# Optimization experiments

Hardware: AMD Instinct MI355X
Metric: run time of the kernel (lower is better)

## Reference

```python
import jax, jax.numpy as jnp
import numpy as np

B, C, H, W = 8, 128, 128, 128

def setup_inputs() -> dict:
    key = jax.random.key(0)
    ks = jax.random.split(key, 6)
    s = 1.0 / np.sqrt(C)
    return {
        "x": jax.random.normal(ks[0], (B, C, H, W), dtype=jnp.float32),
        "w_qkv": jax.random.uniform(ks[1], (3 * C, C), jnp.float32, -s, s),
        "w_gate": jax.random.uniform(ks[2], (C, C), jnp.float32, -s, s),
        "b_gate": jax.random.uniform(ks[3], (C,), jnp.float32, -s, s),
        "w_proj": jax.random.uniform(ks[4], (C, C), jnp.float32, -s, s),
        "b_proj": jax.random.uniform(ks[5], (C,), jnp.float32, -s, s),
    }

def reference(x, w_qkv, w_gate, b_gate, w_proj, b_proj):
    b, c, h, w = x.shape
    n = h * w
    # [b,c,h,w] -> [b,n,c]
    x_seq = jnp.transpose(x, (0, 2, 3, 1)).reshape(b, n, c)
    # SiLU gate on spatial-domain features
    t = jax.nn.silu(x_seq @ w_gate.T + b_gate)  # [b,n,c]
    x_sp = x_seq.reshape(b, h, w, c)
    # frequency domain (ortho norm carries the 1/N factor)
    x_fft = jnp.fft.rfft2(x_sp, axes=(1, 2), norm="ortho")  # [b,h,w//2+1,c] complex64
    # complex linear with real weight == apply weight to real & imag parts
    qkv = jnp.einsum("bhwc,dc->bhwd", x_fft, w_qkv.astype(x_fft.dtype))
    q, k, v = jnp.split(qkv, 3, axis=-1)
    # eq.15: a = F^{-1}(conj(F(Q)) * F(K))
    attn = jnp.fft.irfft2(jnp.conj(q) * k, s=(h, w), axes=(1, 2), norm="ortho")
    # softmax over the flattened spatial axis n
    attn = jax.nn.softmax(attn.reshape(b, n, c), axis=1).reshape(b, h, w, c)
    # eq.16: O = F^{-1}(conj(F(sigma(a))) * F(V)); note forward rfft2 uses default (backward) norm
    attn_f = jnp.fft.rfft2(attn, axes=(1, 2))
    out = jnp.fft.irfft2(jnp.conj(attn_f) * v, s=(h, w), axes=(1, 2), norm="ortho")
    out = out.reshape(b, n, c) * t
    out = out @ w_proj.T + b_proj
    return jnp.transpose(out.reshape(b, h, w, c), (0, 3, 1, 2))
```

## Files before the change

### kernel.cpp

```cpp
#include <hip/hip_runtime.h>
#include <math.h>


constexpr int CH    = 128;
constexpr int NSP   = 128 * 128;
constexpr int BATCH = 8;
constexpr int NIMG  = BATCH * CH;
constexpr int RS    = 130;
constexpr int NT    = 1024;
constexpr int NW    = NT / 64;


typedef short short8 __attribute__((ext_vector_type(8)));
typedef float f32x4  __attribute__((ext_vector_type(4)));
union U8 { unsigned u[4]; short8 s; };

__device__ __forceinline__ unsigned bf16r(float x) {
  unsigned u = __float_as_uint(x);
  return (u + 0x7FFFu + ((u >> 16) & 1u)) >> 16;
}
__device__ __forceinline__ float bflo(unsigned w) { return __uint_as_float(w << 16); }
__device__ __forceinline__ float bfhi(unsigned w) { return __uint_as_float(w & 0xFFFF0000u); }

__device__ __forceinline__ void split_pair(float e0, float e1,
                                           unsigned& hi, unsigned& lo) {
  const unsigned u0 = __float_as_uint(e0), u1 = __float_as_uint(e1);
  hi = (u0 >> 16) | (u1 & 0xFFFF0000u);
  const float r0 = e0 - __uint_as_float(u0 & 0xFFFF0000u);
  const float r1 = e1 - __uint_as_float(u1 & 0xFFFF0000u);
  lo = bf16r(r0) | (bf16r(r1) << 16);
}

__device__ __forceinline__ void load_a_frag(const float* wr, short8& ah, short8& al) {
  const float4 wa = *(const float4*)wr;
  const float4 wb = *(const float4*)(wr + 4);
  U8 hi, lo;
  split_pair(wa.x, wa.y, hi.u[0], lo.u[0]);
  split_pair(wa.z, wa.w, hi.u[1], lo.u[1]);
  split_pair(wb.x, wb.y, hi.u[2], lo.u[2]);
  split_pair(wb.z, wb.w, hi.u[3], lo.u[3]);
  ah = hi.s; al = lo.s;
}


__global__ void prep_weights(const float* __restrict__ w_qkv,
                             const float* __restrict__ w_gate,
                             const float* __restrict__ w_proj,
                             short* __restrict__ wpre) {
  const int t = blockIdx.x * 256 + threadIdx.x;
  const int lane = t & 63;
  const int mf   = (t >> 6) & 3;
  const int kg   = (t >> 8) & 3;
  const int mbi  = (t >> 10) & 1;
  const int g    = t >> 11;
  if (g >= 5) return;
  const float* W = (g < 3) ? (w_qkv + (size_t)g * CH * CH)
                           : (g == 3 ? w_gate : w_proj);
  const int row = mbi * 64 + mf * 16 + (lane & 15);
  const int k0  = kg * 32 + (lane >> 4) * 8;
  short8 ah, al;
  load_a_frag(W + (size_t)row * CH + k0, ah, al);
  const size_t base = ((size_t)(g * 2 + mbi) * 16 + kg * 4 + mf) * 1024;
  *(short8*)(wpre + base + lane * 8)       = ah;
  *(short8*)(wpre + base + 512 + lane * 8) = al;
}


__device__ __forceinline__ void mfma_half(const short8* __restrict__ wf,
                                          const short8 bh[4], const short8 bl[4],
                                          f32x4 acc[4][4], int kg, int lane) {
  short8 ah[4], al[4];
#pragma unroll
  for (int mf = 0; mf < 4; ++mf) {
    const short8* p = wf + (kg * 4 + mf) * 128 + lane;
    ah[mf] = p[0];
    al[mf] = p[64];
  }
#pragma unroll
  for (int mf = 0; mf < 4; ++mf)
#pragma unroll
    for (int nf = 0; nf < 4; ++nf)
      acc[mf][nf] = __builtin_amdgcn_mfma_f32_16x16x32_bf16(al[mf], bh[nf], acc[mf][nf], 0, 0, 0);
#pragma unroll
  for (int mf = 0; mf < 4; ++mf)
#pragma unroll
    for (int nf = 0; nf < 4; ++nf)
      acc[mf][nf] = __builtin_amdgcn_mfma_f32_16x16x32_bf16(ah[mf], bl[nf], acc[mf][nf], 0, 0, 0);
#pragma unroll
  for (int mf = 0; mf < 4; ++mf)
#pragma unroll
    for (int nf = 0; nf < 4; ++nf)
      acc[mf][nf] = __builtin_amdgcn_mfma_f32_16x16x32_bf16(ah[mf], bh[nf], acc[mf][nf], 0, 0, 0);
}

__device__ __forceinline__ void mfma_core2(const unsigned* xs,
                                           const short8* __restrict__ wfA,
                                           const short8* __restrict__ wfB,
                                           f32x4 aA[4][4], f32x4 aB[4][4], int tid) {
  const int lane = tid & 63, wid = tid >> 6;
  const int nb = (wid & 1) * 64;
  const int lm = lane & 15, quad = lane >> 4;
#pragma unroll
  for (int kg = 0; kg < 4; ++kg) {
    short8 bh[4], bl[4];
    const int kwb = (kg * 16 + quad * 4) ^ (lm << 2);
#pragma unroll
    for (int nf = 0; nf < 4; ++nf) {
      const unsigned* p = xs + (nb + nf * 16 + lm) * 64 + kwb;
      bh[nf] = *(const short8*)p;
      bl[nf] = *(const short8*)(p + 8192);
    }
    mfma_half(wfA, bh, bl, aA, kg, lane);
    mfma_half(wfB, bh, bl, aB, kg, lane);
  }
}

__device__ __forceinline__ void mfma_core1(const unsigned* xs,
                                           const short8* __restrict__ wf,
                                           f32x4 acc[4][4], int tid) {
  const int lane = tid & 63, wid = tid >> 6;
  const int nb = (wid & 1) * 64;
  const int lm = lane & 15, quad = lane >> 4;
#pragma unroll
  for (int kg = 0; kg < 4; ++kg) {
    short8 bh[4], bl[4];
    const int kwb = (kg * 16 + quad * 4) ^ (lm << 2);
#pragma unroll
    for (int nf = 0; nf < 4; ++nf) {
      const unsigned* p = xs + (nb + nf * 16 + lm) * 64 + kwb;
      bh[nf] = *(const short8*)p;
      bl[nf] = *(const short8*)(p + 8192);
    }
    mfma_half(wf, bh, bl, acc, kg, lane);
  }
}


__global__ __launch_bounds__(256, 2)
void gemm_qkvg(const float* __restrict__ x, const short* __restrict__ wpre,
               const float* __restrict__ b_gate,
               unsigned* __restrict__ QKp, unsigned short* __restrict__ Vp,
               float* __restrict__ Tp) {
  __shared__ __align__(16) unsigned xs[16384];
  __shared__ __align__(16) float bounce[4 * 528];
  const int tid = threadIdx.x;
  const int n0 = blockIdx.x * 128;
  const int b  = blockIdx.y;
  const float* xb = x + (size_t)b * CH * NSP;

  {
    const int tn = tid >> 3;
    const int tk = tid & 7;
#pragma unroll
    for (int i = 0; i < 8; ++i) {
      const int k = 2 * tk + 16 * i;
      const float* p0 = xb + (size_t)k * NSP + n0 + 4 * tn;
      const float4 a = *(const float4*)p0;
      const float4 c = *(const float4*)(p0 + NSP);
      const float a4[4] = {a.x, a.y, a.z, a.w};
      const float c4[4] = {c.x, c.y, c.z, c.w};
      const int kw = tk + 8 * i;
#pragma unroll
      for (int j = 0; j < 4; ++j) {
        const int nn = 4 * tn + j;
        unsigned hi, lo;
        split_pair(a4[j], c4[j], hi, lo);
        const int kws = kw ^ ((nn & 15) << 2);
        xs[nn * 64 + kws] = hi;
        xs[8192 + nn * 64 + kws] = lo;
      }
    }
  }
  __syncthreads();

  const int lane = tid & 63, wid = tid >> 6;
  const int mb = (wid >> 1) * 64, nb = (wid & 1) * 64;
  const int lm = lane & 15, quad = lane >> 4;
  const int mbi = wid >> 1;
  const short8* wp = (const short8*)wpre;
  const short8* wQ = wp + (size_t)(0 * 2 + mbi) * 2048;
  const short8* wK = wp + (size_t)(1 * 2 + mbi) * 2048;
  const short8* wV = wp + (size_t)(2 * 2 + mbi) * 2048;
  const short8* wG = wp + (size_t)(3 * 2 + mbi) * 2048;
  float* const bw = bounce + wid * 528;
  unsigned* const ubw = (unsigned*)bw;

  f32x4 aq[4][4], ak[4][4];
#pragma unroll
  for (int mf = 0; mf < 4; ++mf)
#pragma unroll
    for (int nf = 0; nf < 4; ++nf) { aq[mf][nf] = (f32x4){0,0,0,0}; ak[mf][nf] = (f32x4){0,0,0,0}; }
  mfma_core2(xs, wQ, wK, aq, ak, tid);

#pragma unroll
  for (int mf = 0; mf < 4; ++mf) {
#pragma unroll
    for (int half = 0; half < 2; ++half) {
#pragma unroll
      for (int nn = 0; nn < 2; ++nn) {
        const int nf = half * 2 + nn;
#pragma unroll
        for (int i = 0; i < 4; ++i)
          ubw[(quad * 4 + i) * 33 + nn * 16 + lm] =
              bf16r(aq[mf][nf][i]) | (bf16r(ak[mf][nf][i]) << 16);
      }
#pragma unroll
      for (int j = 0; j < 2; ++j) {
        const int rl = (lane >> 3) + 8 * j;
        const int cl = (lane & 7) * 4;
        const uint4 v = *(const uint4*)(ubw + rl * 33 + cl);
        const int row = mb + mf * 16 + rl;
        *(uint4*)(QKp + ((size_t)b * CH + row) * NSP + n0 + nb + half * 32 + cl) = v;
      }
    }
  }

  f32x4 av[4][4], at[4][4];
#pragma unroll
  for (int mf = 0; mf < 4; ++mf)
#pragma unroll
    for (int nf = 0; nf < 4; ++nf) { av[mf][nf] = (f32x4){0,0,0,0}; at[mf][nf] = (f32x4){0,0,0,0}; }
  mfma_core2(xs, wV, wG, av, at, tid);

#pragma unroll
  for (int mf = 0; mf < 4; ++mf) {
#pragma unroll
    for (int half = 0; half < 2; ++half) {
#pragma unroll
      for (int nn = 0; nn < 2; ++nn) {
        const int nf = half * 2 + nn;
#pragma unroll
        for (int i = 0; i < 4; ++i)
          bw[(quad * 4 + i) * 33 + nn * 16 + lm] = av[mf][nf][i];
      }
#pragma unroll
      for (int j = 0; j < 2; ++j) {
        const int rl = (lane >> 3) + 8 * j;
        const int cl = (lane & 7) * 4;
        const float4 v = *(const float4*)(bw + rl * 33 + cl);
        const int row = mb + mf * 16 + rl;
        uint2 pv;
        pv.x = bf16r(v.x) | (bf16r(v.y) << 16);
        pv.y = bf16r(v.z) | (bf16r(v.w) << 16);
        *(uint2*)(Vp + ((size_t)b * CH + row) * NSP + n0 + nb + half * 32 + cl) = pv;
      }
    }
  }

#pragma unroll
  for (int mf = 0; mf < 4; ++mf) {
#pragma unroll
    for (int half = 0; half < 2; ++half) {
#pragma unroll
      for (int nn = 0; nn < 2; ++nn) {
        const int nf = half * 2 + nn;
#pragma unroll
        for (int i = 0; i < 4; ++i)
          bw[(quad * 4 + i) * 33 + nn * 16 + lm] = at[mf][nf][i];
      }
#pragma unroll
      for (int j = 0; j < 2; ++j) {
        const int rl = (lane >> 3) + 8 * j;
        const int cl = (lane & 7) * 4;
        float4 v = *(const float4*)(bw + rl * 33 + cl);
        const int row = mb + mf * 16 + rl;
        const float bg = b_gate[row];
        float e[4] = {v.x, v.y, v.z, v.w};
#pragma unroll
        for (int q = 0; q < 4; ++q) {
          const float g = e[q] + bg;
          e[q] = g / (1.0f + __expf(-g));
        }
        v = make_float4(e[0], e[1], e[2], e[3]);
        *(float4*)(Tp + ((size_t)b * CH + row) * NSP + n0 + nb + half * 32 + cl) = v;
      }
    }
  }
}


__device__ __forceinline__ void acc_to_bounce(float* bounce, f32x4 acc[4][4], int tid) {
  const int lane = tid & 63, wid = tid >> 6;
  const int mb = (wid >> 1) * 64;
  const int nb = (wid & 1) * 64;
  const int lm = lane & 15, quad = lane >> 4;
#pragma unroll
  for (int mf = 0; mf < 4; ++mf)
#pragma unroll
    for (int nf = 0; nf < 4; ++nf) {
      const int col = nb + nf * 16 + lm;
      const int r0 = mb + mf * 16 + quad * 4;
#pragma unroll
      for (int i = 0; i < 4; ++i)
        bounce[(r0 + i) * 132 + col] = acc[mf][nf][i];
    }
}

__global__ __launch_bounds__(256, 2)
void gemm_proj(const unsigned short* __restrict__ OC, const float* __restrict__ Tn,
               const short* __restrict__ wpre, const float* __restrict__ b_proj,
               float* __restrict__ outp) {
  __shared__ __align__(16) unsigned xs[16896];
  const int tid = threadIdx.x;
  const int n0 = blockIdx.x * 128;
  const int b = blockIdx.y;
  const unsigned short* ob = OC + (size_t)b * CH * NSP;
  const float* tb = Tn + (size_t)b * CH * NSP;

  {
    const int tn = tid >> 3;
    const int tk = tid & 7;
#pragma unroll
    for (int i = 0; i < 8; ++i) {
      const int k = 2 * tk + 16 * i;
      const uint2 ou0 = *(const uint2*)(ob + (size_t)k * NSP + n0 + 4 * tn);
      const uint2 ou1 = *(const uint2*)(ob + (size_t)(k + 1) * NSP + n0 + 4 * tn);
      const float* pt = tb + (size_t)k * NSP + n0 + 4 * tn;
      const float4 t0 = *(const float4*)pt;
      const float4 t1 = *(const float4*)(pt + NSP);
      const float z0[4] = {bflo(ou0.x) * t0.x, bfhi(ou0.x) * t0.y,
                           bflo(ou0.y) * t0.z, bfhi(ou0.y) * t0.w};
      const float z1[4] = {bflo(ou1.x) * t1.x, bfhi(ou1.x) * t1.y,
                           bflo(ou1.y) * t1.z, bfhi(ou1.y) * t1.w};
      const int kw = tk + 8 * i;
#pragma unroll
      for (int j = 0; j < 4; ++j) {
        const int nn = 4 * tn + j;
        unsigned hi, lo;
        split_pair(z0[j], z1[j], hi, lo);
        const int kws = kw ^ ((nn & 15) << 2);
        xs[nn * 64 + kws] = hi;
        xs[8192 + nn * 64 + kws] = lo;
      }
    }
  }
  __syncthreads();

  const int mbi = (tid >> 6) >> 1;
  const short8* wP = (const short8*)wpre + (size_t)(4 * 2 + mbi) * 2048;

  f32x4 acc[4][4];
#pragma unroll
  for (int mf = 0; mf < 4; ++mf)
#pragma unroll
    for (int nf = 0; nf < 4; ++nf) acc[mf][nf] = (f32x4){0,0,0,0};

  mfma_core1(xs, wP, acc, tid);

  __syncthreads();
  float* bounce = (float*)xs;
  acc_to_bounce(bounce, acc, tid);
  __syncthreads();

  const int rr = tid >> 5;
  const int c4i = (tid & 31) * 4;
#pragma unroll
  for (int i = 0; i < 16; ++i) {
    const int row = rr + 8 * i;
    const float bp = b_proj[row];
    float4 v = *(const float4*)(bounce + row * 132 + c4i);
    v.x += bp; v.y += bp; v.z += bp; v.w += bp;
    *(float4*)(outp + ((size_t)b * CH + row) * NSP + n0 + c4i) = v;
  }
}


__device__ __forceinline__ float2 cmul(float2 a, float2 b) {
  return make_float2(fmaf(a.x, b.x, -(a.y * b.y)), fmaf(a.x, b.y, a.y * b.x));
}
#define CADD(a,b) make_float2((a).x+(b).x,(a).y+(b).y)
#define CSUB(a,b) make_float2((a).x-(b).x,(a).y-(b).y)
#define MULNI(t)  make_float2((t).y, -(t).x)
constexpr float C45 = 0.7071067811865476f;

__device__ __forceinline__ void fft8(float2* x) {
  float2 t;
  t = CSUB(x[0],x[4]); x[0]=CADD(x[0],x[4]); x[4]=t;
  t = CSUB(x[1],x[5]); x[1]=CADD(x[1],x[5]); x[5]=make_float2(C45*(t.x+t.y), C45*(t.y-t.x));
  t = CSUB(x[2],x[6]); x[2]=CADD(x[2],x[6]); x[6]=MULNI(t);
  t = CSUB(x[3],x[7]); x[3]=CADD(x[3],x[7]); x[7]=make_float2(C45*(t.y-t.x), -C45*(t.x+t.y));
  t = CSUB(x[0],x[2]); x[0]=CADD(x[0],x[2]); x[2]=t;
  t = CSUB(x[1],x[3]); x[1]=CADD(x[1],x[3]); x[3]=MULNI(t);
  t = CSUB(x[4],x[6]); x[4]=CADD(x[4],x[6]); x[6]=t;
  t = CSUB(x[5],x[7]); x[5]=CADD(x[5],x[7]); x[7]=MULNI(t);
  t = CSUB(x[0],x[1]); x[0]=CADD(x[0],x[1]); x[1]=t;
  t = CSUB(x[2],x[3]); x[2]=CADD(x[2],x[3]); x[3]=t;
  t = CSUB(x[4],x[5]); x[4]=CADD(x[4],x[5]); x[5]=t;
  t = CSUB(x[6],x[7]); x[6]=CADD(x[6],x[7]); x[7]=t;
}

__device__ __forceinline__ void fft16(float2* z) {
  float2 t;
  t=CSUB(z[0],z[8]);   z[0]=CADD(z[0],z[8]);   z[8]=t;
  t=CSUB(z[1],z[9]);   z[1]=CADD(z[1],z[9]);   z[9]=cmul(t,  make_float2( 0.9238795325f,-0.3826834324f));
  t=CSUB(z[2],z[10]);  z[2]=CADD(z[2],z[10]);  z[10]=make_float2(C45*(t.x+t.y), C45*(t.y-t.x));
  t=CSUB(z[3],z[11]);  z[3]=CADD(z[3],z[11]);  z[11]=cmul(t, make_float2( 0.3826834324f,-0.9238795325f));
  t=CSUB(z[4],z[12]);  z[4]=CADD(z[4],z[12]);  z[12]=MULNI(t);
  t=CSUB(z[5],z[13]);  z[5]=CADD(z[5],z[13]);  z[13]=cmul(t, make_float2(-0.3826834324f,-0.9238795325f));
  t=CSUB(z[6],z[14]);  z[6]=CADD(z[6],z[14]);  z[14]=make_float2(C45*(t.y-t.x), -C45*(t.x+t.y));
  t=CSUB(z[7],z[15]);  z[7]=CADD(z[7],z[15]);  z[15]=cmul(t, make_float2(-0.9238795325f,-0.3826834324f));
  t=CSUB(z[0],z[4]);   z[0]=CADD(z[0],z[4]);   z[4]=t;
  t=CSUB(z[1],z[5]);   z[1]=CADD(z[1],z[5]);   z[5]=make_float2(C45*(t.x+t.y), C45*(t.y-t.x));
  t=CSUB(z[2],z[6]);   z[2]=CADD(z[2],z[6]);   z[6]=MULNI(t);
  t=CSUB(z[3],z[7]);   z[3]=CADD(z[3],z[7]);   z[7]=make_float2(C45*(t.y-t.x), -C45*(t.x+t.y));
  t=CSUB(z[8],z[12]);  z[8]=CADD(z[8],z[12]);  z[12]=t;
  t=CSUB(z[9],z[13]);  z[9]=CADD(z[9],z[13]);  z[13]=make_float2(C45*(t.x+t.y), C45*(t.y-t.x));
  t=CSUB(z[10],z[14]); z[10]=CADD(z[10],z[14]); z[14]=MULNI(t);
  t=CSUB(z[11],z[15]); z[11]=CADD(z[11],z[15]); z[15]=make_float2(C45*(t.y-t.x), -C45*(t.x+t.y));
  t=CSUB(z[0],z[2]);   z[0]=CADD(z[0],z[2]);   z[2]=t;
  t=CSUB(z[1],z[3]);   z[1]=CADD(z[1],z[3]);   z[3]=MULNI(t);
  t=CSUB(z[4],z[6]);   z[4]=CADD(z[4],z[6]);   z[6]=t;
  t=CSUB(z[5],z[7]);   z[5]=CADD(z[5],z[7]);   z[7]=MULNI(t);
  t=CSUB(z[8],z[10]);  z[8]=CADD(z[8],z[10]);  z[10]=t;
  t=CSUB(z[9],z[11]);  z[9]=CADD(z[9],z[11]);  z[11]=MULNI(t);
  t=CSUB(z[12],z[14]); z[12]=CADD(z[12],z[14]); z[14]=t;
  t=CSUB(z[13],z[15]); z[13]=CADD(z[13],z[15]); z[15]=MULNI(t);
  t=CSUB(z[0],z[1]);   z[0]=CADD(z[0],z[1]);   z[1]=t;
  t=CSUB(z[2],z[3]);   z[2]=CADD(z[2],z[3]);   z[3]=t;
  t=CSUB(z[4],z[5]);   z[4]=CADD(z[4],z[5]);   z[5]=t;
  t=CSUB(z[6],z[7]);   z[6]=CADD(z[6],z[7]);   z[7]=t;
  t=CSUB(z[8],z[9]);   z[8]=CADD(z[8],z[9]);   z[9]=t;
  t=CSUB(z[10],z[11]); z[10]=CADD(z[10],z[11]); z[11]=t;
  t=CSUB(z[12],z[13]); z[12]=CADD(z[12],z[13]); z[13]=t;
  t=CSUB(z[14],z[15]); z[14]=CADD(z[14],z[15]); z[15]=t;
}

__device__ __constant__ const float2 WK7[7] = {
  { 0.9987954562f, -0.0490676743f },
  { 0.9951847267f, -0.0980171403f },
  { 0.9891765100f, -0.1467304745f },
  { 0.9807852804f, -0.1950903220f },
  { 0.9700312532f, -0.2429801799f },
  { 0.9569403357f, -0.2902846773f },
  { 0.9415440652f, -0.3368898534f },
};

template<int SRC>
__device__ __forceinline__ void fft_row_pass(float2* img, const float2* twtab,
                                             int lane, int wid,
                                             const unsigned* __restrict__ gqk,
                                             const unsigned short* __restrict__ gv) {
  const int c   = lane & 7;
  const int row = wid * 8 + (lane >> 3);
  const int lb  = RS * row;
  constexpr int br3[8] = {0,4,2,6,1,5,3,7};
  {
    float2 xA[8], xB[8];
    if constexpr (SRC == 0) {
#pragma unroll
      for (int n1 = 0; n1 < 8; ++n1) {
        const float4 v = *(const float4*)(img + lb + 16 * n1 + 2 * c);
        xA[n1] = make_float2(v.x, v.y);
        xB[n1] = make_float2(v.z, v.w);
      }
    } else if constexpr (SRC == 1) {
#pragma unroll
      for (int n1 = 0; n1 < 8; ++n1) {
        const uint2 qk = *(const uint2*)(gqk + row * 128 + 16 * n1 + 2 * c);
        xA[n1] = make_float2(bflo(qk.x), bfhi(qk.x));
        xB[n1] = make_float2(bflo(qk.y), bfhi(qk.y));
      }
    } else {
#pragma unroll
      for (int n1 = 0; n1 < 8; ++n1) {
        const float4 v = *(const float4*)(img + lb + 16 * n1 + 2 * c);
        const unsigned vv = *(const unsigned*)(gv + row * 128 + 16 * n1 + 2 * c);
        xA[n1] = make_float2(v.x, bflo(vv));
        xB[n1] = make_float2(v.z, bfhi(vv));
      }
    }
    fft8(xA); fft8(xB);
#pragma unroll
    for (int m = 0; m < 8; ++m) {
      const int k1 = br3[m];
      float2 yA, yB;
      if (k1 == 0) { yA = xA[m]; yB = xB[m]; }
      else {
        const float2 tA = twtab[(2 * c) * 7 + k1 - 1];
        const float2 tB = cmul(tA, WK7[k1 - 1]);
        yA = cmul(xA[m], tA);
        yB = cmul(xB[m], tB);
      }
      const int d = c ^ (k1 >> 1);
      *(float4*)(img + lb + 16 * k1 + 2 * d) = make_float4(yA.x, yA.y, yB.x, yB.y);
    }
  }
  const int k1 = c;
  float2 z[16];
#pragma unroll
  for (int t = 0; t < 8; ++t) {
    const int u = t ^ (k1 >> 1);
    const float4 v = *(const float4*)(img + lb + 16 * k1 + 2 * u);
    z[2 * t]     = make_float2(v.x, v.y);
    z[2 * t + 1] = make_float2(v.z, v.w);
  }
  fft16(z);
  constexpr int br4[16] = {0,8,4,12,2,10,6,14,1,9,5,13,3,11,7,15};
#pragma unroll
  for (int m = 0; m < 16; ++m)
    img[lb + k1 + 8 * br4[m]] = z[m];
}

template<int EPI>
__device__ __forceinline__ void fft_col_pass(float2* img, const float2* twtab,
                                             int lane, int wid,
                                             float escale, float& lsum) {
  constexpr int br3[8] = {0,4,2,6,1,5,3,7};
  {
    const int n2 = lane & 15;
    const int p  = wid * 4 + (lane >> 4);
    float2 xA[8], xB[8];
#pragma unroll
    for (int n1 = 0; n1 < 8; ++n1) {
      const float4 v = *(const float4*)(img + (16 * n1 + n2) * RS + 2 * p);
      xA[n1] = make_float2(v.x, v.y);
      xB[n1] = make_float2(v.z, v.w);
    }
    fft8(xA); fft8(xB);
#pragma unroll
    for (int m = 0; m < 8; ++m) {
      const int k1m = br3[m];
      float2 yA, yB;
      if (k1m == 0) { yA = xA[m]; yB = xB[m]; }
      else {
        const float2 tw = twtab[n2 * 7 + k1m - 1];
        yA = cmul(xA[m], tw);
        yB = cmul(xB[m], tw);
      }
      *(float4*)(img + (16 * k1m + (n2 ^ k1m)) * RS + 2 * p) = make_float4(yA.x, yA.y, yB.x, yB.y);
    }
  }
  const int k1  = lane & 7;
  const int col = wid * 8 + (lane >> 3);
  float2 z[16];
#pragma unroll
  for (int j = 0; j < 16; ++j) z[j] = img[(16 * k1 + (j ^ k1)) * RS + col];
  fft16(z);
  constexpr int br4[16] = {0,8,4,12,2,10,6,14,1,9,5,13,3,11,7,15};
#pragma unroll
  for (int m = 0; m < 16; ++m) {
    const int a = (k1 + 8 * br4[m]) * RS + col;
    if constexpr (EPI == 1) {
      const float ex = __expf(z[m].x * escale);
      lsum += ex;
      img[a] = make_float2(ex, 0.0f);
    } else {
      img[a] = z[m];
    }
  }
}

__device__ __forceinline__ void cross_spectrum(float2* img, int tid) {
#pragma unroll
  for (int i = 0; i < 8; ++i) {
    const int pid = tid + (i << 10);
    int fr = pid >> 6;
    int fc = pid & 63;
    if (fc == 0) {
      if (fr >= 65) { fc = 64; fr -= 64; }
      else if (fr == 0 || fr == 64) {
        const int a0 = fr * RS;
        const float2 z0 = img[a0];
        img[a0] = make_float2(z0.x * z0.y, 0.0f);
        const int a1 = fr * RS + 64;
        const float2 z1 = img[a1];
        img[a1] = make_float2(z1.x * z1.y, 0.0f);
        continue;
      }
    }
    const int gr = (128 - fr) & 127, gc = (128 - fc) & 127;
    const int f = fr * RS + fc, g = gr * RS + gc;
    const float2 zf = img[f], zg = img[g];
    const float qr = 0.5f * (zf.x + zg.x), qi = 0.5f * (zf.y - zg.y);
    const float kr = 0.5f * (zf.y + zg.y), ki = 0.5f * (zg.x - zf.x);
    const float yr = qr * kr + qi * ki;
    const float yi = qr * ki - qi * kr;
    img[f] = make_float2(yr, -yi);
    img[g] = make_float2(yr, yi);
  }
}

__global__ __launch_bounds__(NT)
void fft_attn_fused(const unsigned* __restrict__ QKin,
                    const unsigned short* __restrict__ Vin,
                    unsigned short* __restrict__ Out) {
  __shared__ __align__(16) float2 img[128 * RS];
  __shared__ __align__(16) float2 twtab[16 * 7];
  __shared__ float red[NW];
  const int tid = threadIdx.x, lane = tid & 63, wid = tid >> 6;
  const size_t off = (size_t)blockIdx.x * NSP;
  const unsigned* gqk = QKin + off;
  const unsigned short* gv = Vin + off;

  if (tid < 112) {
    const int n2 = tid / 7, k = tid % 7 + 1;
    float s, cc;
    sincosf(6.283185307179586f * (1.0f / 128.0f) * (float)(n2 * k), &s, &cc);
    twtab[tid] = make_float2(cc, -s);
  }
  __syncthreads();
  float dummy = 0.0f;

  fft_row_pass<1>(img, twtab, lane, wid, gqk, nullptr);
  __syncthreads();
  fft_col_pass<0>(img, twtab, lane, wid, 0.0f, dummy);
  __syncthreads();
  cross_spectrum(img, tid);
  __syncthreads();
  const float escale = 1.0f / 2097152.0f;
  float lsum = 0.0f;
  fft_row_pass<0>(img, twtab, lane, wid, nullptr, nullptr);
  __syncthreads();
  fft_col_pass<1>(img, twtab, lane, wid, escale, lsum);
  __syncthreads();

#pragma unroll
  for (int s = 32; s >= 1; s >>= 1) lsum += __shfl_xor(lsum, s, 64);
  if (lane == 0) red[wid] = lsum;
  __syncthreads();
  float tot = 0.0f;
#pragma unroll
  for (int w = 0; w < NW; ++w) tot += red[w];
  const float inv = 1.0f / tot;

  fft_row_pass<2>(img, twtab, lane, wid, nullptr, gv);
  __syncthreads();
  fft_col_pass<0>(img, twtab, lane, wid, 0.0f, dummy);
  __syncthreads();
  cross_spectrum(img, tid);
  __syncthreads();
  fft_row_pass<0>(img, twtab, lane, wid, nullptr, nullptr);
  __syncthreads();
  fft_col_pass<0>(img, twtab, lane, wid, 0.0f, dummy);
  __syncthreads();

  const float os = inv * (1.0f / 16384.0f);
#pragma unroll
  for (int i = 0; i < 4; ++i) {
    const int e = (tid + i * NT) * 4;
    const float2* base = img + (e >> 7) * RS + (e & 127);
    const float4 a = *(const float4*)base;
    const float4 c = *(const float4*)(base + 2);
    uint2 o;
    o.x = bf16r(a.x * os) | (bf16r(a.z * os) << 16);
    o.y = bf16r(c.x * os) | (bf16r(c.z * os) << 16);
    *(uint2*)(Out + off + e) = o;
  }
}


extern "C" void kernel_launch(void* const* d_in, const int* in_sizes, int n_in,
                              void* d_out, int out_size, void* d_ws, size_t ws_size,
                              hipStream_t stream) {
  const float* x      = (const float*)d_in[0];
  const float* w_qkv  = (const float*)d_in[1];
  const float* w_gate = (const float*)d_in[2];
  const float* b_gate = (const float*)d_in[3];
  const float* w_proj = (const float*)d_in[4];
  const float* b_proj = (const float*)d_in[5];
  float* outp = (float*)d_out;

  const size_t SZ = (size_t)BATCH * CH * NSP;
  char* base = (char*)d_ws;
  unsigned*       QK = (unsigned*)base;
  unsigned short* V  = (unsigned short*)(base + SZ * 4);
  float*          T  = (float*)(base + SZ * 6);
  unsigned short* OC = (unsigned short*)(base + SZ * 10);
  short*          WP = (short*)(base + SZ * 12);

  prep_weights<<<40, 256, 0, stream>>>(w_qkv, w_gate, w_proj, WP);

  dim3 g1(128, BATCH);
  gemm_qkvg<<<g1, 256, 0, stream>>>(x, WP, b_gate, QK, V, T);

  fft_attn_fused<<<NIMG, NT, 0, stream>>>(QK, V, OC);

  dim3 g2(128, BATCH);
  gemm_proj<<<g2, 256, 0, stream>>>(OC, T, WP, b_proj, outp);
}
```

Baseline: 347.5 us.

## Fuse cross-spectrum computation into inverse row FFT pass with paired row mapping

Removes the standalone cross_spectrum pass and computes the conjugate-product on the fly while loading the inverse row FFT, with rows assigned so each wave handles mirror-row pairs. This removes one full LDS read/write sweep of the 128x130 image and one barrier per attention stage. It also moves the softmax-sum readback to the end of the kernel, dropping the barrier after the exp column pass. The in-place fused read of mirror rows relies on the row-to-wave mapping keeping each row and its mirror inside one wave, so correctness depends on that mapping.

```diff
diff --git a/kernel.cpp b/kernel.cpp
--- a/kernel.cpp
+++ b/kernel.cpp
@@ -435,6 +435,14 @@
   { 0.9415440652f, -0.3368898534f },
 };
 
+__device__ __forceinline__ float2 crossY(float2 zf, float2 zg) {
+  const float qr = 0.5f * (zf.x + zg.x), qi = 0.5f * (zf.y - zg.y);
+  const float kr = 0.5f * (zf.y + zg.y), ki = 0.5f * (zg.x - zf.x);
+  const float yr = qr * kr + qi * ki;
+  const float yi = qr * ki - qi * kr;
+  return make_float2(yr, -yi);
+}
+
 template<int SRC>
 __device__ __forceinline__ void fft_row_pass(float2* img, const float2* twtab,
                                              int lane, int wid,
@@ -446,14 +454,7 @@
   constexpr int br3[8] = {0,4,2,6,1,5,3,7};
   {
     float2 xA[8], xB[8];
-    if constexpr (SRC == 0) {
-#pragma unroll
-      for (int n1 = 0; n1 < 8; ++n1) {
-        const float4 v = *(const float4*)(img + lb + 16 * n1 + 2 * c);
-        xA[n1] = make_float2(v.x, v.y);
-        xB[n1] = make_float2(v.z, v.w);
-      }
-    } else if constexpr (SRC == 1) {
+    if constexpr (SRC == 1) {
 #pragma unroll
       for (int n1 = 0; n1 < 8; ++n1) {
         const uint2 qk = *(const uint2*)(gqk + row * 128 + 16 * n1 + 2 * c);
@@ -501,6 +502,60 @@
     img[lb + k1 + 8 * br4[m]] = z[m];
 }
 
+__device__ __forceinline__ void fft_row_cross(float2* img, const float2* twtab,
+                                              int lane, int wid) {
+  const int c  = lane & 7;
+  const int rg = lane >> 3;
+  const int row = (wid == 0)
+      ? (rg < 4 ? rg : (rg == 4 ? 64 : 120 + rg))
+      : (rg < 4 ? 4 * wid + rg : 132 - 4 * wid - rg);
+  const int mrow = (128 - row) & 127;
+  const int lb = RS * row;
+  const int mb = RS * mrow;
+  constexpr int br3[8] = {0,4,2,6,1,5,3,7};
+  {
+    float2 xA[8], xB[8];
+#pragma unroll
+    for (int n1 = 0; n1 < 8; ++n1) {
+      const int A = 16 * n1 + 2 * c;
+      const float4 v  = *(const float4*)(img + lb + A);
+      const float2 g0 = img[mb + ((128 - A) & 127)];
+      const float2 g1 = img[mb + (127 - A)];
+      xA[n1] = crossY(make_float2(v.x, v.y), g0);
+      xB[n1] = crossY(make_float2(v.z, v.w), g1);
+    }
+    fft8(xA); fft8(xB);
+#pragma unroll
+    for (int m = 0; m < 8; ++m) {
+      const int k1 = br3[m];
+      float2 yA, yB;
+      if (k1 == 0) { yA = xA[m]; yB = xB[m]; }
+      else {
+        const float2 tA = twtab[(2 * c) * 7 + k1 - 1];
+        const float2 tB = cmul(tA, WK7[k1 - 1]);
+        yA = cmul(xA[m], tA);
+        yB = cmul(xB[m], tB);
+      }
+      const int d = c ^ (k1 >> 1);
+      *(float4*)(img + lb + 16 * k1 + 2 * d) = make_float4(yA.x, yA.y, yB.x, yB.y);
+    }
+  }
+  const int k1 = c;
+  float2 z[16];
+#pragma unroll
+  for (int t = 0; t < 8; ++t) {
+    const int u = t ^ (k1 >> 1);
+    const float4 v = *(const float4*)(img + lb + 16 * k1 + 2 * u);
+    z[2 * t]     = make_float2(v.x, v.y);
+    z[2 * t + 1] = make_float2(v.z, v.w);
+  }
+  fft16(z);
+  constexpr int br4[16] = {0,8,4,12,2,10,6,14,1,9,5,13,3,11,7,15};
+#pragma unroll
+  for (int m = 0; m < 16; ++m)
+    img[lb + k1 + 8 * br4[m]] = z[m];
+}
+
 template<int EPI>
 __device__ __forceinline__ void fft_col_pass(float2* img, const float2* twtab,
                                              int lane, int wid,
@@ -547,36 +602,6 @@
     } else {
       img[a] = z[m];
     }
-  }
-}
-
-__device__ __forceinline__ void cross_spectrum(float2* img, int tid) {
-#pragma unroll
-  for (int i = 0; i < 8; ++i) {
-    const int pid = tid + (i << 10);
-    int fr = pid >> 6;
-    int fc = pid & 63;
-    if (fc == 0) {
-      if (fr >= 65) { fc = 64; fr -= 64; }
-      else if (fr == 0 || fr == 64) {
-        const int a0 = fr * RS;
-        const float2 z0 = img[a0];
-        img[a0] = make_float2(z0.x * z0.y, 0.0f);
-        const int a1 = fr * RS + 64;
-        const float2 z1 = img[a1];
-        img[a1] = make_float2(z1.x * z1.y, 0.0f);
-        continue;
-      }
-    }
-    const int gr = (128 - fr) & 127, gc = (128 - fc) & 127;
-    const int f = fr * RS + fc, g = gr * RS + gc;
-    const float2 zf = img[f], zg = img[g];
-    const float qr = 0.5f * (zf.x + zg.x), qi = 0.5f * (zf.y - zg.y);
-    const float kr = 0.5f * (zf.y + zg.y), ki = 0.5f * (zg.x - zf.x);
-    const float yr = qr * kr + qi * ki;
-    const float yi = qr * ki - qi * kr;
-    img[f] = make_float2(yr, -yi);
-    img[g] = make_float2(yr, yi);
   }
 }
 
@@ -605,36 +630,29 @@
   __syncthreads();
   fft_col_pass<0>(img, twtab, lane, wid, 0.0f, dummy);
   __syncthreads();
-  cross_spectrum(img, tid);
-  __syncthreads();
   const float escale = 1.0f / 2097152.0f;
+  fft_row_cross(img, twtab, lane, wid);
+  __syncthreads();
   float lsum = 0.0f;
-  fft_row_pass<0>(img, twtab, lane, wid, nullptr, nullptr);
-  __syncthreads();
   fft_col_pass<1>(img, twtab, lane, wid, escale, lsum);
-  __syncthreads();
-
 #pragma unroll
   for (int s = 32; s >= 1; s >>= 1) lsum += __shfl_xor(lsum, s, 64);
   if (lane == 0) red[wid] = lsum;
   __syncthreads();
+
+  fft_row_pass<2>(img, twtab, lane, wid, nullptr, gv);
+  __syncthreads();
+  fft_col_pass<0>(img, twtab, lane, wid, 0.0f, dummy);
+  __syncthreads();
+  fft_row_cross(img, twtab, lane, wid);
+  __syncthreads();
+  fft_col_pass<0>(img, twtab, lane, wid, 0.0f, dummy);
+  __syncthreads();
+
   float tot = 0.0f;
 #pragma unroll
   for (int w = 0; w < NW; ++w) tot += red[w];
-  const float inv = 1.0f / tot;
-
-  fft_row_pass<2>(img, twtab, lane, wid, nullptr, gv);
-  __syncthreads();
-  fft_col_pass<0>(img, twtab, lane, wid, 0.0f, dummy);
-  __syncthreads();
-  cross_spectrum(img, tid);
-  __syncthreads();
-  fft_row_pass<0>(img, twtab, lane, wid, nullptr, nullptr);
-  __syncthreads();
-  fft_col_pass<0>(img, twtab, lane, wid, 0.0f, dummy);
-  __syncthreads();
-
-  const float os = inv * (1.0f / 16384.0f);
+  const float os = (1.0f / tot) * (1.0f / 16384.0f);
 #pragma unroll
   for (int i = 0; i < 4; ++i) {
     const int e = (tid + i * NT) * 4;
```

Measured after the change: 371.8 us. +7.0%, slower.

## Use 512-thread GEMM blocks with 8 waves and remove an FFT barrier

Applied to the files above, without the earlier changes.

Both GEMM kernels now run with 512 threads (8 waves) per block. Each wave computes a 64x32 output tile instead of 64x64, which halves accumulator registers per wave and adds latency hiding within the block. The staging loads and the LDS bounce buffers are reshaped to fit the new wave layout. In the FFT kernel, the softmax-sum reduction is moved so that one __syncthreads is dropped and the read of the reduced total is deferred past the second FFT chain. In exchange, each wave reuses its weight fragments across fewer columns, so LDS and weight-load traffic per MFMA goes up.

```diff
diff --git a/kernel.cpp b/kernel.cpp
--- a/kernel.cpp
+++ b/kernel.cpp
@@ -66,9 +66,9 @@
 }
 
 
-__device__ __forceinline__ void mfma_half(const short8* __restrict__ wf,
-                                          const short8 bh[4], const short8 bl[4],
-                                          f32x4 acc[4][4], int kg, int lane) {
+__device__ __forceinline__ void mfma_half2(const short8* __restrict__ wf,
+                                           const short8 bh[2], const short8 bl[2],
+                                           f32x4 acc[4][2], int kg, int lane) {
   short8 ah[4], al[4];
 #pragma unroll
   for (int mf = 0; mf < 4; ++mf) {
@@ -79,87 +79,84 @@
 #pragma unroll
   for (int mf = 0; mf < 4; ++mf)
 #pragma unroll
-    for (int nf = 0; nf < 4; ++nf)
+    for (int nf = 0; nf < 2; ++nf)
       acc[mf][nf] = __builtin_amdgcn_mfma_f32_16x16x32_bf16(al[mf], bh[nf], acc[mf][nf], 0, 0, 0);
 #pragma unroll
   for (int mf = 0; mf < 4; ++mf)
 #pragma unroll
-    for (int nf = 0; nf < 4; ++nf)
+    for (int nf = 0; nf < 2; ++nf)
       acc[mf][nf] = __builtin_amdgcn_mfma_f32_16x16x32_bf16(ah[mf], bl[nf], acc[mf][nf], 0, 0, 0);
 #pragma unroll
   for (int mf = 0; mf < 4; ++mf)
 #pragma unroll
-    for (int nf = 0; nf < 4; ++nf)
+    for (int nf = 0; nf < 2; ++nf)
       acc[mf][nf] = __builtin_amdgcn_mfma_f32_16x16x32_bf16(ah[mf], bh[nf], acc[mf][nf], 0, 0, 0);
 }
 
-__device__ __forceinline__ void mfma_core2(const unsigned* xs,
-                                           const short8* __restrict__ wfA,
-                                           const short8* __restrict__ wfB,
-                                           f32x4 aA[4][4], f32x4 aB[4][4], int tid) {
-  const int lane = tid & 63, wid = tid >> 6;
-  const int nb = (wid & 1) * 64;
+__device__ __forceinline__ void mfma_core2x(const unsigned* xs,
+                                            const short8* __restrict__ wfA,
+                                            const short8* __restrict__ wfB,
+                                            f32x4 aA[4][2], f32x4 aB[4][2],
+                                            int lane, int nb) {
   const int lm = lane & 15, quad = lane >> 4;
 #pragma unroll
   for (int kg = 0; kg < 4; ++kg) {
-    short8 bh[4], bl[4];
+    short8 bh[2], bl[2];
     const int kwb = (kg * 16 + quad * 4) ^ (lm << 2);
 #pragma unroll
-    for (int nf = 0; nf < 4; ++nf) {
+    for (int nf = 0; nf < 2; ++nf) {
       const unsigned* p = xs + (nb + nf * 16 + lm) * 64 + kwb;
       bh[nf] = *(const short8*)p;
       bl[nf] = *(const short8*)(p + 8192);
     }
-    mfma_half(wfA, bh, bl, aA, kg, lane);
-    mfma_half(wfB, bh, bl, aB, kg, lane);
-  }
-}
-
-__device__ __forceinline__ void mfma_core1(const unsigned* xs,
-                                           const short8* __restrict__ wf,
-                                           f32x4 acc[4][4], int tid) {
-  const int lane = tid & 63, wid = tid >> 6;
-  const int nb = (wid & 1) * 64;
+    mfma_half2(wfA, bh, bl, aA, kg, lane);
+    mfma_half2(wfB, bh, bl, aB, kg, lane);
+  }
+}
+
+__device__ __forceinline__ void mfma_core1x(const unsigned* xs,
+                                            const short8* __restrict__ wf,
+                                            f32x4 acc[4][2], int lane, int nb) {
   const int lm = lane & 15, quad = lane >> 4;
 #pragma unroll
   for (int kg = 0; kg < 4; ++kg) {
-    short8 bh[4], bl[4];
+    short8 bh[2], bl[2];
     const int kwb = (kg * 16 + quad * 4) ^ (lm << 2);
 #pragma unroll
-    for (int nf = 0; nf < 4; ++nf) {
+    for (int nf = 0; nf < 2; ++nf) {
       const unsigned* p = xs + (nb + nf * 16 + lm) * 64 + kwb;
       bh[nf] = *(const short8*)p;
       bl[nf] = *(const short8*)(p + 8192);
     }
-    mfma_half(wf, bh, bl, acc, kg, lane);
-  }
-}
-
-
-__global__ __launch_bounds__(256, 2)
+    mfma_half2(wf, bh, bl, acc, kg, lane);
+  }
+}
+
+
+__global__ __launch_bounds__(512, 4)
 void gemm_qkvg(const float* __restrict__ x, const short* __restrict__ wpre,
                const float* __restrict__ b_gate,
                unsigned* __restrict__ QKp, unsigned short* __restrict__ Vp,
                float* __restrict__ Tp) {
   __shared__ __align__(16) unsigned xs[16384];
-  __shared__ __align__(16) float bounce[4 * 528];
+  __shared__ __align__(16) unsigned bounce[8 * 272];
   const int tid = threadIdx.x;
   const int n0 = blockIdx.x * 128;
   const int b  = blockIdx.y;
   const float* xb = x + (size_t)b * CH * NSP;
 
   {
-    const int tn = tid >> 3;
-    const int tk = tid & 7;
-#pragma unroll
-    for (int i = 0; i < 8; ++i) {
-      const int k = 2 * tk + 16 * i;
+    const int tn = tid >> 4;
+    const int tk = tid & 15;
+#pragma unroll
+    for (int i = 0; i < 4; ++i) {
+      const int k = 2 * tk + 32 * i;
       const float* p0 = xb + (size_t)k * NSP + n0 + 4 * tn;
       const float4 a = *(const float4*)p0;
       const float4 c = *(const float4*)(p0 + NSP);
       const float a4[4] = {a.x, a.y, a.z, a.w};
       const float c4[4] = {c.x, c.y, c.z, c.w};
-      const int kw = tk + 8 * i;
+      const int kw = tk + 16 * i;
 #pragma unroll
       for (int j = 0; j < 4; ++j) {
         const int nn = 4 * tn + j;
@@ -174,129 +171,88 @@
   __syncthreads();
 
   const int lane = tid & 63, wid = tid >> 6;
-  const int mb = (wid >> 1) * 64, nb = (wid & 1) * 64;
+  const int mbi = wid >> 2;
+  const int mb  = mbi * 64;
+  const int nb  = (wid & 3) * 32;
   const int lm = lane & 15, quad = lane >> 4;
-  const int mbi = wid >> 1;
   const short8* wp = (const short8*)wpre;
   const short8* wQ = wp + (size_t)(0 * 2 + mbi) * 2048;
   const short8* wK = wp + (size_t)(1 * 2 + mbi) * 2048;
   const short8* wV = wp + (size_t)(2 * 2 + mbi) * 2048;
   const short8* wG = wp + (size_t)(3 * 2 + mbi) * 2048;
-  float* const bw = bounce + wid * 528;
-  unsigned* const ubw = (unsigned*)bw;
-
-  f32x4 aq[4][4], ak[4][4];
+  unsigned* const ubw = bounce + wid * 272;
+  float* const fbw = (float*)ubw;
+  const int rl = lane >> 2;
+  const int cl = (lane & 3) * 4;
+
+  f32x4 aq[4][2], ak[4][2];
 #pragma unroll
   for (int mf = 0; mf < 4; ++mf)
 #pragma unroll
-    for (int nf = 0; nf < 4; ++nf) { aq[mf][nf] = (f32x4){0,0,0,0}; ak[mf][nf] = (f32x4){0,0,0,0}; }
-  mfma_core2(xs, wQ, wK, aq, ak, tid);
+    for (int nf = 0; nf < 2; ++nf) { aq[mf][nf] = (f32x4){0,0,0,0}; ak[mf][nf] = (f32x4){0,0,0,0}; }
+  mfma_core2x(xs, wQ, wK, aq, ak, lane, nb);
 
 #pragma unroll
   for (int mf = 0; mf < 4; ++mf) {
 #pragma unroll
-    for (int half = 0; half < 2; ++half) {
-#pragma unroll
-      for (int nn = 0; nn < 2; ++nn) {
-        const int nf = half * 2 + nn;
-#pragma unroll
-        for (int i = 0; i < 4; ++i)
-          ubw[(quad * 4 + i) * 33 + nn * 16 + lm] =
-              bf16r(aq[mf][nf][i]) | (bf16r(ak[mf][nf][i]) << 16);
-      }
-#pragma unroll
-      for (int j = 0; j < 2; ++j) {
-        const int rl = (lane >> 3) + 8 * j;
-        const int cl = (lane & 7) * 4;
-        const uint4 v = *(const uint4*)(ubw + rl * 33 + cl);
-        const int row = mb + mf * 16 + rl;
-        *(uint4*)(QKp + ((size_t)b * CH + row) * NSP + n0 + nb + half * 32 + cl) = v;
-      }
-    }
-  }
-
-  f32x4 av[4][4], at[4][4];
+    for (int nf = 0; nf < 2; ++nf) {
+#pragma unroll
+      for (int i = 0; i < 4; ++i)
+        ubw[(quad * 4 + i) * 17 + lm] =
+            bf16r(aq[mf][nf][i]) | (bf16r(ak[mf][nf][i]) << 16);
+      const uint4 v = *(const uint4*)(ubw + rl * 17 + cl);
+      const int row = mb + mf * 16 + rl;
+      *(uint4*)(QKp + ((size_t)b * CH + row) * NSP + n0 + nb + nf * 16 + cl) = v;
+    }
+  }
+
+  f32x4 av[4][2], at[4][2];
 #pragma unroll
   for (int mf = 0; mf < 4; ++mf)
 #pragma unroll
-    for (int nf = 0; nf < 4; ++nf) { av[mf][nf] = (f32x4){0,0,0,0}; at[mf][nf] = (f32x4){0,0,0,0}; }
-  mfma_core2(xs, wV, wG, av, at, tid);
+    for (int nf = 0; nf < 2; ++nf) { av[mf][nf] = (f32x4){0,0,0,0}; at[mf][nf] = (f32x4){0,0,0,0}; }
+  mfma_core2x(xs, wV, wG, av, at, lane, nb);
 
 #pragma unroll
   for (int mf = 0; mf < 4; ++mf) {
 #pragma unroll
-    for (int half = 0; half < 2; ++half) {
-#pragma unroll
-      for (int nn = 0; nn < 2; ++nn) {
-        const int nf = half * 2 + nn;
-#pragma unroll
-        for (int i = 0; i < 4; ++i)
-          bw[(quad * 4 + i) * 33 + nn * 16 + lm] = av[mf][nf][i];
-      }
-#pragma unroll
-      for (int j = 0; j < 2; ++j) {
-        const int rl = (lane >> 3) + 8 * j;
-        const int cl = (lane & 7) * 4;
-        const float4 v = *(const float4*)(bw + rl * 33 + cl);
-        const int row = mb + mf * 16 + rl;
-        uint2 pv;
-        pv.x = bf16r(v.x) | (bf16r(v.y) << 16);
-        pv.y = bf16r(v.z) | (bf16r(v.w) << 16);
-        *(uint2*)(Vp + ((size_t)b * CH + row) * NSP + n0 + nb + half * 32 + cl) = pv;
-      }
+    for (int nf = 0; nf < 2; ++nf) {
+#pragma unroll
+      for (int i = 0; i < 4; ++i)
+        fbw[(quad * 4 + i) * 17 + lm] = av[mf][nf][i];
+      const float4 v = *(const float4*)(fbw + rl * 17 + cl);
+      const int row = mb + mf * 16 + rl;
+      uint2 pv;
+      pv.x = bf16r(v.x) | (bf16r(v.y) << 16);
+      pv.y = bf16r(v.z) | (bf16r(v.w) << 16);
+      *(uint2*)(Vp + ((size_t)b * CH + row) * NSP + n0 + nb + nf * 16 + cl) = pv;
     }
   }
 
 #pragma unroll
   for (int mf = 0; mf < 4; ++mf) {
 #pragma unroll
-    for (int half = 0; half < 2; ++half) {
-#pragma unroll
-      for (int nn = 0; nn < 2; ++nn) {
-        const int nf = half * 2 + nn;
-#pragma unroll
-        for (int i = 0; i < 4; ++i)
-          bw[(quad * 4 + i) * 33 + nn * 16 + lm] = at[mf][nf][i];
-      }
-#pragma unroll
-      for (int j = 0; j < 2; ++j) {
-        const int rl = (lane >> 3) + 8 * j;
-        const int cl = (lane & 7) * 4;
-        float4 v = *(const float4*)(bw + rl * 33 + cl);
-        const int row = mb + mf * 16 + rl;
-        const float bg = b_gate[row];
-        float e[4] = {v.x, v.y, v.z, v.w};
-#pragma unroll
-        for (int q = 0; q < 4; ++q) {
-          const float g = e[q] + bg;
-          e[q] = g / (1.0f + __expf(-g));
-        }
-        v = make_float4(e[0], e[1], e[2], e[3]);
-        *(float4*)(Tp + ((size_t)b * CH + row) * NSP + n0 + nb + half * 32 + cl) = v;
-      }
-    }
-  }
-}
-
-
-__device__ __forceinline__ void acc_to_bounce(float* bounce, f32x4 acc[4][4], int tid) {
-  const int lane = tid & 63, wid = tid >> 6;
-  const int mb = (wid >> 1) * 64;
-  const int nb = (wid & 1) * 64;
-  const int lm = lane & 15, quad = lane >> 4;
-#pragma unroll
-  for (int mf = 0; mf < 4; ++mf)
-#pragma unroll
-    for (int nf = 0; nf < 4; ++nf) {
-      const int col = nb + nf * 16 + lm;
-      const int r0 = mb + mf * 16 + quad * 4;
+    for (int nf = 0; nf < 2; ++nf) {
 #pragma unroll
       for (int i = 0; i < 4; ++i)
-        bounce[(r0 + i) * 132 + col] = acc[mf][nf][i];
-    }
-}
-
-__global__ __launch_bounds__(256, 2)
+        fbw[(quad * 4 + i) * 17 + lm] = at[mf][nf][i];
+      float4 v = *(const float4*)(fbw + rl * 17 + cl);
+      const int row = mb + mf * 16 + rl;
+      const float bg = b_gate[row];
+      float e[4] = {v.x, v.y, v.z, v.w};
+#pragma unroll
+      for (int q = 0; q < 4; ++q) {
+        const float g = e[q] + bg;
+        e[q] = g / (1.0f + __expf(-g));
+      }
+      v = make_float4(e[0], e[1], e[2], e[3]);
+      *(float4*)(Tp + ((size_t)b * CH + row) * NSP + n0 + nb + nf * 16 + cl) = v;
+    }
+  }
+}
+
+
+__global__ __launch_bounds__(512, 4)
 void gemm_proj(const unsigned short* __restrict__ OC, const float* __restrict__ Tn,
                const short* __restrict__ wpre, const float* __restrict__ b_proj,
                float* __restrict__ outp) {
@@ -308,11 +264,11 @@
   const float* tb = Tn + (size_t)b * CH * NSP;
 
   {
-    const int tn = tid >> 3;
-    const int tk = tid & 7;
-#pragma unroll
-    for (int i = 0; i < 8; ++i) {
-      const int k = 2 * tk + 16 * i;
+    const int tn = tid >> 4;
+    const int tk = tid & 15;
+#pragma unroll
+    for (int i = 0; i < 4; ++i) {
+      const int k = 2 * tk + 32 * i;
       const uint2 ou0 = *(const uint2*)(ob + (size_t)k * NSP + n0 + 4 * tn);
       const uint2 ou1 = *(const uint2*)(ob + (size_t)(k + 1) * NSP + n0 + 4 * tn);
       const float* pt = tb + (size_t)k * NSP + n0 + 4 * tn;
@@ -322,7 +278,7 @@
                            bflo(ou0.y) * t0.z, bfhi(ou0.y) * t0.w};
       const float z1[4] = {bflo(ou1.x) * t1.x, bfhi(ou1.x) * t1.y,
                            bflo(ou1.y) * t1.z, bfhi(ou1.y) * t1.w};
-      const int kw = tk + 8 * i;
+      const int kw = tk + 16 * i;
 #pragma unroll
       for (int j = 0; j < 4; ++j) {
         const int nn = 4 * tn + j;
@@ -336,27 +292,40 @@
   }
   __syncthreads();
 
-  const int mbi = (tid >> 6) >> 1;
+  const int lane = tid & 63, wid = tid >> 6;
+  const int mbi = wid >> 2;
+  const int mb  = mbi * 64;
+  const int nb  = (wid & 3) * 32;
+  const int lm = lane & 15, quad = lane >> 4;
   const short8* wP = (const short8*)wpre + (size_t)(4 * 2 + mbi) * 2048;
 
-  f32x4 acc[4][4];
+  f32x4 acc[4][2];
 #pragma unroll
   for (int mf = 0; mf < 4; ++mf)
 #pragma unroll
-    for (int nf = 0; nf < 4; ++nf) acc[mf][nf] = (f32x4){0,0,0,0};
-
-  mfma_core1(xs, wP, acc, tid);
+    for (int nf = 0; nf < 2; ++nf) acc[mf][nf] = (f32x4){0,0,0,0};
+
+  mfma_core1x(xs, wP, acc, lane, nb);
 
   __syncthreads();
   float* bounce = (float*)xs;
-  acc_to_bounce(bounce, acc, tid);
+#pragma unroll
+  for (int mf = 0; mf < 4; ++mf)
+#pragma unroll
+    for (int nf = 0; nf < 2; ++nf) {
+      const int col = nb + nf * 16 + lm;
+      const int r0 = mb + mf * 16 + quad * 4;
+#pragma unroll
+      for (int i = 0; i < 4; ++i)
+        bounce[(r0 + i) * 132 + col] = acc[mf][nf][i];
+    }
   __syncthreads();
 
   const int rr = tid >> 5;
   const int c4i = (tid & 31) * 4;
 #pragma unroll
-  for (int i = 0; i < 16; ++i) {
-    const int row = rr + 8 * i;
+  for (int i = 0; i < 8; ++i) {
+    const int row = rr + 16 * i;
     const float bp = b_proj[row];
     float4 v = *(const float4*)(bounce + row * 132 + c4i);
     v.x += bp; v.y += bp; v.z += bp; v.w += bp;
@@ -612,29 +581,26 @@
   fft_row_pass<0>(img, twtab, lane, wid, nullptr, nullptr);
   __syncthreads();
   fft_col_pass<1>(img, twtab, lane, wid, escale, lsum);
-  __syncthreads();
-
 #pragma unroll
   for (int s = 32; s >= 1; s >>= 1) lsum += __shfl_xor(lsum, s, 64);
   if (lane == 0) red[wid] = lsum;
   __syncthreads();
+
+  fft_row_pass<2>(img, twtab, lane, wid, nullptr, gv);
+  __syncthreads();
+  fft_col_pass<0>(img, twtab, lane, wid, 0.0f, dummy);
+  __syncthreads();
+  cross_spectrum(img, tid);
+  __syncthreads();
+  fft_row_pass<0>(img, twtab, lane, wid, nullptr, nullptr);
+  __syncthreads();
+  fft_col_pass<0>(img, twtab, lane, wid, 0.0f, dummy);
+  __syncthreads();
+
   float tot = 0.0f;
 #pragma unroll
   for (int w = 0; w < NW; ++w) tot += red[w];
-  const float inv = 1.0f / tot;
-
-  fft_row_pass<2>(img, twtab, lane, wid, nullptr, gv);
-  __syncthreads();
-  fft_col_pass<0>(img, twtab, lane, wid, 0.0f, dummy);
-  __syncthreads();
-  cross_spectrum(img, tid);
-  __syncthreads();
-  fft_row_pass<0>(img, twtab, lane, wid, nullptr, nullptr);
-  __syncthreads();
-  fft_col_pass<0>(img, twtab, lane, wid, 0.0f, dummy);
-  __syncthreads();
-
-  const float os = inv * (1.0f / 16384.0f);
+  const float os = (1.0f / tot) * (1.0f / 16384.0f);
 #pragma unroll
   for (int i = 0; i < 4; ++i) {
     const int e = (tid + i * NT) * 4;
@@ -671,10 +637,10 @@
   prep_weights<<<40, 256, 0, stream>>>(w_qkv, w_gate, w_proj, WP);
 
   dim3 g1(128, BATCH);
-  gemm_qkvg<<<g1, 256, 0, stream>>>(x, WP, b_gate, QK, V, T);
+  gemm_qkvg<<<g1, 512, 0, stream>>>(x, WP, b_gate, QK, V, T);
 
   fft_attn_fused<<<NIMG, NT, 0, stream>>>(QK, V, OC);
 
   dim3 g2(128, BATCH);
-  gemm_proj<<<g2, 256, 0, stream>>>(OC, T, WP, b_proj, outp);
-}
+  gemm_proj<<<g2, 512, 0, stream>>>(OC, T, WP, b_proj, outp);
+}
```

Result: slower. 434.2 us (+25.0%).
